# Kernel optimization log

Hardware: AMD Instinct MI355X
Metric: run time of the kernel (lower is better)

## Reference

```python
import jax, jax.numpy as jnp
import numpy as np

B, T, D_IN = 256, 2048, 64
H1, H2, D_OUT = 256, 256, 2


def setup_inputs() -> dict:
    key = jax.random.key(0)
    ks = jax.random.split(key, 12)
    s = lambda fan_in: 1.0 / np.sqrt(fan_in)
    u = lambda k, shape, b: jax.random.uniform(k, shape, jnp.float32, -b, b)
    return {
        "input_tensor": jax.random.normal(ks[0], (B, T, D_IN), jnp.float32),
        # layer 0 LSTMCell params (torch layout: [4H, in], gate order i,f,g,o)
        "W_ih0": u(ks[1], (4 * H1, D_IN), s(H1)),
        "W_hh0": u(ks[2], (4 * H1, H1), s(H1)),
        "b_ih0": u(ks[3], (4 * H1,), s(H1)),
        "b_hh0": u(ks[4], (4 * H1,), s(H1)),
        # layer 1 LSTMCell params
        "W_ih1": u(ks[5], (4 * H2, H1), s(H2)),
        "W_hh1": u(ks[6], (4 * H2, H2), s(H2)),
        "b_ih1": u(ks[7], (4 * H2,), s(H2)),
        "b_hh1": u(ks[8], (4 * H2,), s(H2)),
        # dense head
        "W_dense": u(ks[9], (D_OUT, H2), s(H2)),
        "b_dense": u(ks[10], (D_OUT,), s(H2)),
    }


def _lstm_cell(x, h, c, W_ih, W_hh, b_ih, b_hh):
    # gates: [B, 4H]; torch gate order i, f, g, o
    g = x @ W_ih.T + h @ W_hh.T + (b_ih + b_hh)
    i, f, gg, o = jnp.split(g, 4, axis=-1)
    c_new = jax.nn.sigmoid(f) * c + jax.nn.sigmoid(i) * jnp.tanh(gg)
    h_new = jax.nn.sigmoid(o) * jnp.tanh(c_new)
    return h_new, c_new


def reference(input_tensor, W_ih0, W_hh0, b_ih0, b_hh0,
              W_ih1, W_hh1, b_ih1, b_hh1, W_dense, b_dense):
    b = input_tensor.shape[0]
    h0 = jnp.zeros((b, H1), input_tensor.dtype)
    c0 = jnp.zeros((b, H1), input_tensor.dtype)
    h1 = jnp.zeros((b, H2), input_tensor.dtype)
    c1 = jnp.zeros((b, H2), input_tensor.dtype)

    def step(carry, x_t):
        h0, c0, h1, c1 = carry
        h0, c0 = _lstm_cell(x_t, h0, c0, W_ih0, W_hh0, b_ih0, b_hh0)
        h1, c1 = _lstm_cell(h0, h1, c1, W_ih1, W_hh1, b_ih1, b_hh1)
        return (h0, c0, h1, c1), None

    xs = jnp.swapaxes(input_tensor, 0, 1)  # [T, B, D_IN]
    (h0, c0, h1, c1), _ = jax.lax.scan(step, (h0, c0, h1, c1), xs)
    # dropout_rate=0.0 -> identity; final_act_type='none' -> identity
    out = h1 @ W_dense.T + b_dense  # [B, D_OUT]
    return out
```

## Files before the change

### kernel.cpp

```cpp
#include <hip/hip_runtime.h>
#include <math.h>

#define TT 2048
#define DIN 64
#define HH 256

typedef __attribute__((ext_vector_type(8))) short bf16x8;
typedef __attribute__((ext_vector_type(4))) float f32x4;
typedef __attribute__((ext_vector_type(4))) unsigned u32x4;
typedef unsigned short u16;
typedef unsigned u32t;

#define XS_STR 72
#define HS_STR 264
#define GB_STR 36

#define OFF_XS_HI  0
#define OFF_XS_LO  (OFF_XS_HI + 32*XS_STR)
#define OFF_HS0_HI (OFF_XS_LO + 32*XS_STR)
#define OFF_HS0_LO (OFF_HS0_HI + 32*HS_STR)
#define OFF_HS1_HI (OFF_HS0_LO + 32*HS_STR)
#define OFF_HS1_LO (OFF_HS1_HI + 32*HS_STR)
#define OFF_W0LO   (OFF_HS1_LO + 32*HS_STR)
#define OFF_W1LO   (OFF_W0LO + 1280*8)
#define SH_SHORTS  (OFF_W1LO + 2048*8)
#define SH_BYTES   (SH_SHORTS*2)
#define LDS_BYTES  (SH_BYTES + 2368*4)

__device__ __forceinline__ u16 f2bf(float f){
    u32t u = __builtin_bit_cast(u32t, f);
    u += 0x7fffu + ((u >> 16) & 1u);
    return (u16)(u >> 16);
}
__device__ __forceinline__ float bf2f(u16 h){
    u32t u = ((u32t)h) << 16;
    return __builtin_bit_cast(float, u);
}
__device__ __forceinline__ float sigf(float v){ return 1.0f/(1.0f+__expf(-v)); }
__device__ __forceinline__ float tanh_fast(float v){
    float x = fminf(fmaxf(v, -20.f), 20.f);
    float t = __expf(2.f*x);
    return (t - 1.f) / (t + 1.f);
}

__device__ __forceinline__ void split8(float4 a, float4 b, bf16x8& hi, bf16x8& lo){
    float v[8] = {a.x,a.y,a.z,a.w,b.x,b.y,b.z,b.w};
    #pragma unroll
    for (int j=0;j<8;++j){
        u16 h = f2bf(v[j]);
        hi[j] = (short)h;
        lo[j] = (short)f2bf(v[j] - bf2f(h));
    }
}

__device__ __forceinline__ void group_barrier(u32t* flg, int ug, unsigned epoch){
    __syncthreads();
    if (threadIdx.x == 0){
        asm volatile("s_waitcnt vmcnt(0)" ::: "memory");
        *(volatile u32t*)(flg + ug*16) = epoch;
    }
    if (threadIdx.x < 32){
        while (*(volatile u32t*)(flg + threadIdx.x*16) < epoch)
            __builtin_amdgcn_s_sleep(1);
    }
    __syncthreads();
}

#define MFMA16(a,b,c_) __builtin_amdgcn_mfma_f32_16x16x32_bf16(a,b,c_,0,0,0)

__global__ __launch_bounds__(256, 1)
void lstm_v8(const float* __restrict__ x,
             const float* __restrict__ Wih0, const float* __restrict__ Whh0,
             const float* __restrict__ bih0, const float* __restrict__ bhh0,
             const float* __restrict__ Wih1, const float* __restrict__ Whh1,
             const float* __restrict__ bih1, const float* __restrict__ bhh1,
             const float* __restrict__ Wd,   const float* __restrict__ bd,
             float* __restrict__ out, u16* __restrict__ hb,
             u32t* __restrict__ flags)
{
    extern __shared__ char smem[];
    short* sh  = (short*)smem;
    float* sf  = (float*)(smem + SH_BYTES);
    float* gb0 = sf;
    float* gb1 = sf + 1152;
    float* b0s = sf + 2304;
    float* b1s = sf + 2336;

    const int tid = threadIdx.x;
    const int w   = blockIdx.x;
    const int rb  = w & 7;
    const int ug  = w >> 3;
    const int rbase = rb * 32;
    const int u0  = ug * 8;

    u32t* flg = flags + rb * 512;


    const int l  = tid & 63;
    const int wv = tid >> 6;
    const int mt = wv >> 1, nt = wv & 1;
    const int c  = l & 15, ks = l >> 4;
    const int gbx = nt*2 + (c >> 3);
    const int g   = gbx*HH + u0 + (c & 7);

    bf16x8 w0h[10];
    #pragma unroll
    for (int kt = 0; kt < 10; ++kt) {
        int k = kt*32 + ks*8;
        const float* p = (k < 64) ? (Wih0 + (size_t)g*64 + k)
                                  : (Whh0 + (size_t)g*HH + (k - 64));
        bf16x8 hi_, lo_;
        split8(*(const float4*)p, *(const float4*)(p+4), hi_, lo_);
        w0h[kt] = hi_;
    }
    bf16x8 w1h[16];
    #pragma unroll
    for (int kt = 0; kt < 16; ++kt) {
        int k = kt*32 + ks*8;
        const float* p = (k < 256) ? (Wih1 + (size_t)g*HH + k)
                                   : (Whh1 + (size_t)g*HH + (k - 256));
        bf16x8 hi_, lo_;
        split8(*(const float4*)p, *(const float4*)(p+4), hi_, lo_);
        w1h[kt] = hi_;
    }
    for (int f = tid; f < 1280; f += 256) {
        int c_ = f & 15, ks_ = (f>>4)&3, nt_ = (f>>6)&1, kt_ = f>>7;
        int g_ = (nt_*2 + (c_>>3))*HH + u0 + (c_&7);
        int k_ = kt_*32 + ks_*8;
        const float* p = (k_ < 64) ? (Wih0 + (size_t)g_*64 + k_)
                                   : (Whh0 + (size_t)g_*HH + (k_ - 64));
        bf16x8 hi_, lo_;
        split8(*(const float4*)p, *(const float4*)(p+4), hi_, lo_);
        *(bf16x8*)(sh + OFF_W0LO + f*8) = lo_;
    }
    for (int f = tid; f < 2048; f += 256) {
        int c_ = f & 15, ks_ = (f>>4)&3, nt_ = (f>>6)&1, kt_ = f>>7;
        int g_ = (nt_*2 + (c_>>3))*HH + u0 + (c_&7);
        int k_ = kt_*32 + ks_*8;
        const float* p = (k_ < 256) ? (Wih1 + (size_t)g_*HH + k_)
                                    : (Whh1 + (size_t)g_*HH + (k_ - 256));
        bf16x8 hi_, lo_;
        split8(*(const float4*)p, *(const float4*)(p+4), hi_, lo_);
        *(bf16x8*)(sh + OFF_W1LO + f*8) = lo_;
    }

    if (tid < 32) {
        int gg_ = (tid >> 3)*HH + u0 + (tid & 7);
        b0s[tid] = bih0[gg_] + bhh0[gg_];
        b1s[tid] = bih1[gg_] + bhh1[gg_];
    }
    {
        int zr = tid >> 3, zu = tid & 7;
        size_t off = (size_t)(rbase + zr)*HH + u0 + zu;
        *(volatile u16*)(hb + off) = 0;          *(volatile u16*)(hb + 65536 + off) = 0;
        *(volatile u16*)(hb + 131072 + off) = 0; *(volatile u16*)(hb + 196608 + off) = 0;
        *(volatile u16*)(hb + 262144 + off) = 0; *(volatile u16*)(hb + 327680 + off) = 0;
        *(volatile u16*)(hb + 393216 + off) = 0; *(volatile u16*)(hb + 458752 + off) = 0;
    }
    {
        int xr = tid >> 3, xk = (tid & 7)*8;
        const float* xp = x + (size_t)(rbase + xr)*(TT*DIN) + xk;
        bf16x8 xh, xl;
        split8(*(const float4*)xp, *(const float4*)(xp+4), xh, xl);
        *(bf16x8*)(sh + OFF_XS_HI + xr*XS_STR + xk) = xh;
        *(bf16x8*)(sh + OFF_XS_LO + xr*XS_STR + xk) = xl;
    }
    group_barrier(flg, ug, 1u);

    const short* axh = sh + OFF_XS_HI  + (mt*16 + c)*XS_STR + ks*8;
    const short* axl = sh + OFF_XS_LO  + (mt*16 + c)*XS_STR + ks*8;
    const short* a0h = sh + OFF_HS0_HI + (mt*16 + c)*HS_STR + ks*8;
    const short* a0l = sh + OFF_HS0_LO + (mt*16 + c)*HS_STR + ks*8;
    const short* a1h = sh + OFF_HS1_HI + (mt*16 + c)*HS_STR + ks*8;
    const short* a1l = sh + OFF_HS1_LO + (mt*16 + c)*HS_STR + ks*8;
    const short* b0lo = sh + OFF_W0LO + (nt*64 + ks*16 + c)*8;
    const short* b1lo = sh + OFF_W1LO + (nt*64 + ks*16 + c)*8;
    float* gw0 = gb0 + (mt*16 + ks*4)*GB_STR + nt*16 + c;
    float* gw1 = gb1 + (mt*16 + ks*4)*GB_STR + nt*16 + c;
    const int ur = tid >> 3, uu = tid & 7;
    const size_t poff = (size_t)(rbase + ur)*HH + u0 + uu;

    float c0s = 0.f, c1s = 0.f;

    for (int k = 0; k <= TT; ++k) {
        {
            const unsigned rdo = ((k + 1) & 1) * 65536u;
            const u16* s0h = hb + rdo;
            const u16* s0l = hb + 131072 + rdo;
            const u16* s1h = hb + 262144 + rdo;
            const u16* s1l = hb + 393216 + rdo;
            #pragma unroll
            for (int j = 0; j < 4; ++j) {
                int cid = tid + j*256;
                int hr = cid >> 5, hk = (cid & 31)*8;
                size_t goff = (size_t)(rbase + hr)*HH + hk;
                int loff = hr*HS_STR + hk;
                *(u32x4*)(sh + OFF_HS0_HI + loff) = *(const volatile u32x4*)(s0h + goff);
                *(u32x4*)(sh + OFF_HS0_LO + loff) = *(const volatile u32x4*)(s0l + goff);
                *(u32x4*)(sh + OFF_HS1_HI + loff) = *(const volatile u32x4*)(s1h + goff);
                *(u32x4*)(sh + OFF_HS1_LO + loff) = *(const volatile u32x4*)(s1l + goff);
            }
        }
        __syncthreads();

        if (k < TT) {
            f32x4 ac[4] = {};
            #pragma unroll
            for (int kt = 0; kt < 10; ++kt) {
                const short* ph = (kt < 2) ? (axh + kt*32) : (a0h + (kt-2)*32);
                const short* pl = (kt < 2) ? (axl + kt*32) : (a0l + (kt-2)*32);
                bf16x8 ah = *(const bf16x8*)ph;
                bf16x8 al = *(const bf16x8*)pl;
                bf16x8 wl = *(const bf16x8*)(b0lo + kt*1024);
                const int q = kt & 3;
                ac[q] = MFMA16(ah, w0h[kt], ac[q]);
                ac[q] = MFMA16(al, w0h[kt], ac[q]);
                ac[q] = MFMA16(ah, wl,      ac[q]);
            }
            f32x4 aa = (ac[0] + ac[1]) + (ac[2] + ac[3]);
            gw0[0]        = aa[0];
            gw0[GB_STR]   = aa[1];
            gw0[2*GB_STR] = aa[2];
            gw0[3*GB_STR] = aa[3];
        }
        if (k >= 1) {
            f32x4 ac[4] = {};
            #pragma unroll
            for (int kt = 0; kt < 16; ++kt) {
                const short* ph = (kt < 8) ? (a0h + kt*32) : (a1h + (kt-8)*32);
                const short* pl = (kt < 8) ? (a0l + kt*32) : (a1l + (kt-8)*32);
                bf16x8 ah = *(const bf16x8*)ph;
                bf16x8 al = *(const bf16x8*)pl;
                bf16x8 wl = *(const bf16x8*)(b1lo + kt*1024);
                const int q = kt & 3;
                ac[q] = MFMA16(ah, w1h[kt], ac[q]);
                ac[q] = MFMA16(al, w1h[kt], ac[q]);
                ac[q] = MFMA16(ah, wl,      ac[q]);
            }
            f32x4 aa = (ac[0] + ac[1]) + (ac[2] + ac[3]);
            gw1[0]        = aa[0];
            gw1[GB_STR]   = aa[1];
            gw1[2*GB_STR] = aa[2];
            gw1[3*GB_STR] = aa[3];
        }
        __syncthreads();

        const unsigned wro = (k & 1) * 65536u;
        if (k < TT) {
            float gi = gb0[ur*GB_STR + uu]      + b0s[uu];
            float gf = gb0[ur*GB_STR + 8 + uu]  + b0s[8+uu];
            float gg = gb0[ur*GB_STR + 16 + uu] + b0s[16+uu];
            float go = gb0[ur*GB_STR + 24 + uu] + b0s[24+uu];
            c0s = sigf(gf)*c0s + sigf(gi)*tanh_fast(gg);
            float hn = sigf(go)*tanh_fast(c0s);
            u16 hh_ = f2bf(hn);
            u16 hl_ = f2bf(hn - bf2f(hh_));
            *(volatile u16*)(hb + wro + poff)          = hh_;
            *(volatile u16*)(hb + 131072 + wro + poff) = hl_;
        }
        if (k >= 1) {
            float gi = gb1[ur*GB_STR + uu]      + b1s[uu];
            float gf = gb1[ur*GB_STR + 8 + uu]  + b1s[8+uu];
            float gg = gb1[ur*GB_STR + 16 + uu] + b1s[16+uu];
            float go = gb1[ur*GB_STR + 24 + uu] + b1s[24+uu];
            c1s = sigf(gf)*c1s + sigf(gi)*tanh_fast(gg);
            float hn = sigf(go)*tanh_fast(c1s);
            u16 hh_ = f2bf(hn);
            u16 hl_ = f2bf(hn - bf2f(hh_));
            *(volatile u16*)(hb + 262144 + wro + poff) = hh_;
            *(volatile u16*)(hb + 393216 + wro + poff) = hl_;
        }
        if (k + 1 < TT) {
            int xr = tid >> 3, xk = (tid & 7)*8;
            const float* xp = x + (size_t)(rbase + xr)*(TT*DIN) + (size_t)(k+1)*DIN + xk;
            bf16x8 xh, xl;
            split8(*(const float4*)xp, *(const float4*)(xp+4), xh, xl);
            *(bf16x8*)(sh + OFF_XS_HI + xr*XS_STR + xk) = xh;
            *(bf16x8*)(sh + OFF_XS_LO + xr*XS_STR + xk) = xl;
        }
        group_barrier(flg, ug, (unsigned)(k+2));
    }

    if (ug == 0 && tid < 64) {
        int r = tid >> 1, j = tid & 1;
        const u16* hhp = hb + 262144 + (size_t)(rbase + r)*HH;
        const u16* hlp = hb + 393216 + (size_t)(rbase + r)*HH;
        const float* wdp = Wd + j*HH;
        float a = bd[j];
        #pragma unroll 4
        for (int q = 0; q < HH; ++q)
            a += (bf2f(*(const volatile u16*)(hhp + q)) +
                  bf2f(*(const volatile u16*)(hlp + q))) * wdp[q];
        out[(rbase + r)*2 + j] = a;
    }
}

extern "C" void kernel_launch(void* const* d_in, const int* in_sizes, int n_in,
                              void* d_out, int out_size, void* d_ws, size_t ws_size,
                              hipStream_t stream) {
    const float* x    = (const float*)d_in[0];
    const float* Wih0 = (const float*)d_in[1];
    const float* Whh0 = (const float*)d_in[2];
    const float* bih0 = (const float*)d_in[3];
    const float* bhh0 = (const float*)d_in[4];
    const float* Wih1 = (const float*)d_in[5];
    const float* Whh1 = (const float*)d_in[6];
    const float* bih1 = (const float*)d_in[7];
    const float* bhh1 = (const float*)d_in[8];
    const float* Wd   = (const float*)d_in[9];
    const float* bd   = (const float*)d_in[10];
    float* out = (float*)d_out;

    u32t* flags = (u32t*)d_ws;
    u16* hb = (u16*)((char*)d_ws + 32768);

    hipMemsetAsync(d_ws, 0, 32768, stream);

    hipFuncSetAttribute((const void*)lstm_v8,
                        hipFuncAttributeMaxDynamicSharedMemorySize, LDS_BYTES);

    lstm_v8<<<dim3(256), dim3(256), LDS_BYTES, stream>>>(
        x, Wih0, Whh0, bih0, bhh0, Wih1, Whh1, bih1, bhh1,
        Wd, bd, out, hb, flags);
}
```

Before: 17.00 ms.

## Use fragment-ordered hidden-state exchange layout, register-resident layer-1 weights, atomic barrier

```diff
diff --git a/kernel.cpp b/kernel.cpp
--- a/kernel.cpp
+++ b/kernel.cpp
@@ -11,21 +11,15 @@
 typedef unsigned short u16;
 typedef unsigned u32t;
 
-#define XS_STR 72
-#define HS_STR 264
-#define GB_STR 36
-
-#define OFF_XS_HI  0
-#define OFF_XS_LO  (OFF_XS_HI + 32*XS_STR)
-#define OFF_HS0_HI (OFF_XS_LO + 32*XS_STR)
-#define OFF_HS0_LO (OFF_HS0_HI + 32*HS_STR)
-#define OFF_HS1_HI (OFF_HS0_LO + 32*HS_STR)
-#define OFF_HS1_LO (OFF_HS1_HI + 32*HS_STR)
-#define OFF_W0LO   (OFF_HS1_LO + 32*HS_STR)
-#define OFF_W1LO   (OFF_W0LO + 1280*8)
-#define SH_SHORTS  (OFF_W1LO + 2048*8)
-#define SH_BYTES   (SH_SHORTS*2)
-#define LDS_BYTES  (SH_BYTES + 2368*4)
+#define LH0HI 0
+#define LH0LO 8192
+#define LH1HI 16384
+#define LH1LO 24576
+#define LX    32768
+#define LW0LO 40960
+#define SH_SHORTS 51200
+#define SH_BYTES (SH_SHORTS*2)
+#define LDS_BYTES (SH_BYTES + 2176*4)
 
 __device__ __forceinline__ u16 f2bf(float f){
     u32t u = __builtin_bit_cast(u32t, f);
@@ -42,7 +36,6 @@
     float t = __expf(2.f*x);
     return (t - 1.f) / (t + 1.f);
 }
-
 __device__ __forceinline__ void split8(float4 a, float4 b, bf16x8& hi, bf16x8& lo){
     float v[8] = {a.x,a.y,a.z,a.w,b.x,b.y,b.z,b.w};
     #pragma unroll
@@ -55,12 +48,10 @@
 
 __device__ __forceinline__ void group_barrier(u32t* flg, int ug, unsigned epoch){
     __syncthreads();
-    if (threadIdx.x == 0){
-        asm volatile("s_waitcnt vmcnt(0)" ::: "memory");
-        *(volatile u32t*)(flg + ug*16) = epoch;
-    }
+    if (threadIdx.x == 0)
+        __hip_atomic_store(flg + ug*16, epoch, __ATOMIC_RELEASE, __HIP_MEMORY_SCOPE_AGENT);
     if (threadIdx.x < 32){
-        while (*(volatile u32t*)(flg + threadIdx.x*16) < epoch)
+        while (__hip_atomic_load(flg + threadIdx.x*16, __ATOMIC_ACQUIRE, __HIP_MEMORY_SCOPE_AGENT) < epoch)
             __builtin_amdgcn_s_sleep(1);
     }
     __syncthreads();
@@ -69,22 +60,22 @@
 #define MFMA16(a,b,c_) __builtin_amdgcn_mfma_f32_16x16x32_bf16(a,b,c_,0,0,0)
 
 __global__ __launch_bounds__(256, 1)
-void lstm_v8(const float* __restrict__ x,
-             const float* __restrict__ Wih0, const float* __restrict__ Whh0,
-             const float* __restrict__ bih0, const float* __restrict__ bhh0,
-             const float* __restrict__ Wih1, const float* __restrict__ Whh1,
-             const float* __restrict__ bih1, const float* __restrict__ bhh1,
-             const float* __restrict__ Wd,   const float* __restrict__ bd,
-             float* __restrict__ out, u16* __restrict__ hb,
-             u32t* __restrict__ flags)
+void lstm_v11(const float* __restrict__ x,
+              const float* __restrict__ Wih0, const float* __restrict__ Whh0,
+              const float* __restrict__ bih0, const float* __restrict__ bhh0,
+              const float* __restrict__ Wih1, const float* __restrict__ Whh1,
+              const float* __restrict__ bih1, const float* __restrict__ bhh1,
+              const float* __restrict__ Wd,   const float* __restrict__ bd,
+              float* __restrict__ out, u16* __restrict__ hb,
+              u32t* __restrict__ flags)
 {
     extern __shared__ char smem[];
     short* sh  = (short*)smem;
     float* sf  = (float*)(smem + SH_BYTES);
-    float* gb0 = sf;
-    float* gb1 = sf + 1152;
-    float* b0s = sf + 2304;
-    float* b1s = sf + 2336;
+    float* gbT0 = sf;
+    float* gbT1 = sf + 1056;
+    float* b0s  = sf + 2112;
+    float* b1s  = sf + 2144;
 
     const int tid = threadIdx.x;
     const int w   = blockIdx.x;
@@ -95,6 +86,7 @@
 
     u32t* flg = flags + rb * 512;
 
+    u16* gbase = hb + (size_t)rb * 65536;
 
     const int l  = tid & 63;
     const int wv = tid >> 6;
@@ -105,112 +97,95 @@
 
     bf16x8 w0h[10];
     #pragma unroll
-    for (int kt = 0; kt < 10; ++kt) {
+    for (int kt = 0; kt < 10; ++kt){
         int k = kt*32 + ks*8;
-        const float* p = (k < 64) ? (Wih0 + (size_t)g*64 + k)
+        const float* p = (k < 64) ? (Wih0 + (size_t)g*DIN + k)
                                   : (Whh0 + (size_t)g*HH + (k - 64));
-        bf16x8 hi_, lo_;
-        split8(*(const float4*)p, *(const float4*)(p+4), hi_, lo_);
+        bf16x8 hi_, lo_; split8(*(const float4*)p, *(const float4*)(p+4), hi_, lo_);
         w0h[kt] = hi_;
     }
-    bf16x8 w1h[16];
+    bf16x8 w1h[16], w1l[16];
     #pragma unroll
-    for (int kt = 0; kt < 16; ++kt) {
+    for (int kt = 0; kt < 16; ++kt){
         int k = kt*32 + ks*8;
         const float* p = (k < 256) ? (Wih1 + (size_t)g*HH + k)
                                    : (Whh1 + (size_t)g*HH + (k - 256));
-        bf16x8 hi_, lo_;
-        split8(*(const float4*)p, *(const float4*)(p+4), hi_, lo_);
-        w1h[kt] = hi_;
-    }
-    for (int f = tid; f < 1280; f += 256) {
+        bf16x8 hi_, lo_; split8(*(const float4*)p, *(const float4*)(p+4), hi_, lo_);
+        w1h[kt] = hi_; w1l[kt] = lo_;
+    }
+    for (int f = tid; f < 1280; f += 256){
         int c_ = f & 15, ks_ = (f>>4)&3, nt_ = (f>>6)&1, kt_ = f>>7;
         int g_ = (nt_*2 + (c_>>3))*HH + u0 + (c_&7);
         int k_ = kt_*32 + ks_*8;
-        const float* p = (k_ < 64) ? (Wih0 + (size_t)g_*64 + k_)
+        const float* p = (k_ < 64) ? (Wih0 + (size_t)g_*DIN + k_)
                                    : (Whh0 + (size_t)g_*HH + (k_ - 64));
-        bf16x8 hi_, lo_;
-        split8(*(const float4*)p, *(const float4*)(p+4), hi_, lo_);
-        *(bf16x8*)(sh + OFF_W0LO + f*8) = lo_;
-    }
-    for (int f = tid; f < 2048; f += 256) {
-        int c_ = f & 15, ks_ = (f>>4)&3, nt_ = (f>>6)&1, kt_ = f>>7;
-        int g_ = (nt_*2 + (c_>>3))*HH + u0 + (c_&7);
-        int k_ = kt_*32 + ks_*8;
-        const float* p = (k_ < 256) ? (Wih1 + (size_t)g_*HH + k_)
-                                    : (Whh1 + (size_t)g_*HH + (k_ - 256));
-        bf16x8 hi_, lo_;
-        split8(*(const float4*)p, *(const float4*)(p+4), hi_, lo_);
-        *(bf16x8*)(sh + OFF_W1LO + f*8) = lo_;
-    }
-
-    if (tid < 32) {
-        int gg_ = (tid >> 3)*HH + u0 + (tid & 7);
+        bf16x8 hi_, lo_; split8(*(const float4*)p, *(const float4*)(p+4), hi_, lo_);
+        *(bf16x8*)(sh + LW0LO + f*8) = lo_;
+    }
+
+    if (tid < 32){
+        int gg_ = ((tid>>4)*2 + ((tid>>3)&1))*HH + u0 + (tid & 7);
         b0s[tid] = bih0[gg_] + bhh0[gg_];
         b1s[tid] = bih1[gg_] + bhh1[gg_];
     }
     {
-        int zr = tid >> 3, zu = tid & 7;
-        size_t off = (size_t)(rbase + zr)*HH + u0 + zu;
-        *(volatile u16*)(hb + off) = 0;          *(volatile u16*)(hb + 65536 + off) = 0;
-        *(volatile u16*)(hb + 131072 + off) = 0; *(volatile u16*)(hb + 196608 + off) = 0;
-        *(volatile u16*)(hb + 262144 + off) = 0; *(volatile u16*)(hb + 327680 + off) = 0;
-        *(volatile u16*)(hb + 393216 + off) = 0; *(volatile u16*)(hb + 458752 + off) = 0;
+        int idx = ug*256 + tid;
+        u32x4 z = {0u,0u,0u,0u};
+        *(u32x4*)(gbase + (size_t)idx*8) = z;
     }
     {
-        int xr = tid >> 3, xk = (tid & 7)*8;
-        const float* xp = x + (size_t)(rbase + xr)*(TT*DIN) + xk;
-        bf16x8 xh, xl;
-        split8(*(const float4*)xp, *(const float4*)(xp+4), xh, xl);
-        *(bf16x8*)(sh + OFF_XS_HI + xr*XS_STR + xk) = xh;
-        *(bf16x8*)(sh + OFF_XS_LO + xr*XS_STR + xk) = xl;
+        int xr = tid >> 3, k8 = tid & 7;
+        const float* xp = x + (size_t)(rbase + xr)*(TT*DIN) + k8*8;
+        bf16x8 xh, xl; split8(*(const float4*)xp, *(const float4*)(xp+4), xh, xl);
+        short* d = sh + LX + (k8>>2)*1024 + (xr>>4)*512
+                 + (((k8&3) ^ (xr&3))<<7) + (xr&15)*8;
+        *(bf16x8*)d = xh;
+        *(bf16x8*)(d + 2048) = xl;
     }
     group_barrier(flg, ug, 1u);
 
-    const short* axh = sh + OFF_XS_HI  + (mt*16 + c)*XS_STR + ks*8;
-    const short* axl = sh + OFF_XS_LO  + (mt*16 + c)*XS_STR + ks*8;
-    const short* a0h = sh + OFF_HS0_HI + (mt*16 + c)*HS_STR + ks*8;
-    const short* a0l = sh + OFF_HS0_LO + (mt*16 + c)*HS_STR + ks*8;
-    const short* a1h = sh + OFF_HS1_HI + (mt*16 + c)*HS_STR + ks*8;
-    const short* a1l = sh + OFF_HS1_LO + (mt*16 + c)*HS_STR + ks*8;
-    const short* b0lo = sh + OFF_W0LO + (nt*64 + ks*16 + c)*8;
-    const short* b1lo = sh + OFF_W1LO + (nt*64 + ks*16 + c)*8;
-    float* gw0 = gb0 + (mt*16 + ks*4)*GB_STR + nt*16 + c;
-    float* gw1 = gb1 + (mt*16 + ks*4)*GB_STR + nt*16 + c;
+    const int hoff = mt*512 + l*8;
+    const int xoff = mt*512 + ((ks ^ (c&3))<<7) + c*8;
+    const short* b0lo = sh + LW0LO + (nt*64 + ks*16 + c)*8;
+    float* gw0 = gbT0 + (nt*16 + c)*33 + mt*16 + ks*4;
+    float* gw1 = gbT1 + (nt*16 + c)*33 + mt*16 + ks*4;
+
     const int ur = tid >> 3, uu = tid & 7;
-    const size_t poff = (size_t)(rbase + ur)*HH + u0 + uu;
+    const int fpub = (ug>>2)*1024 + (ur>>4)*512 + ((ug&3)<<7) + (ur&15)*8 + uu;
 
     float c0s = 0.f, c1s = 0.f;
 
-    for (int k = 0; k <= TT; ++k) {
+    for (int k = 0; k <= TT; ++k){
         {
-            const unsigned rdo = ((k + 1) & 1) * 65536u;
-            const u16* s0h = hb + rdo;
-            const u16* s0l = hb + 131072 + rdo;
-            const u16* s1h = hb + 262144 + rdo;
-            const u16* s1l = hb + 393216 + rdo;
+            const int p = (k + 1) & 1;
+            const u16* s0h = gbase + (0 + p)*8192;
+            const u16* s0l = gbase + (2 + p)*8192;
+            const u16* s1h = gbase + (4 + p)*8192;
+            const u16* s1l = gbase + (6 + p)*8192;
             #pragma unroll
-            for (int j = 0; j < 4; ++j) {
-                int cid = tid + j*256;
-                int hr = cid >> 5, hk = (cid & 31)*8;
-                size_t goff = (size_t)(rbase + hr)*HH + hk;
-                int loff = hr*HS_STR + hk;
-                *(u32x4*)(sh + OFF_HS0_HI + loff) = *(const volatile u32x4*)(s0h + goff);
-                *(u32x4*)(sh + OFF_HS0_LO + loff) = *(const volatile u32x4*)(s0l + goff);
-                *(u32x4*)(sh + OFF_HS1_HI + loff) = *(const volatile u32x4*)(s1h + goff);
-                *(u32x4*)(sh + OFF_HS1_LO + loff) = *(const volatile u32x4*)(s1l + goff);
+            for (int j = 0; j < 4; ++j){
+                int idx = (tid + j*256) * 8;
+                *(u32x4*)(sh + LH0HI + idx) = *(const u32x4*)(s0h + idx);
+                *(u32x4*)(sh + LH0LO + idx) = *(const u32x4*)(s0l + idx);
+                *(u32x4*)(sh + LH1HI + idx) = *(const u32x4*)(s1h + idx);
+                *(u32x4*)(sh + LH1LO + idx) = *(const u32x4*)(s1l + idx);
             }
         }
         __syncthreads();
 
-        if (k < TT) {
+        if (k < TT){
             f32x4 ac[4] = {};
+            const short* xb = sh + LX + (k&1)*4096 + xoff;
             #pragma unroll
-            for (int kt = 0; kt < 10; ++kt) {
-                const short* ph = (kt < 2) ? (axh + kt*32) : (a0h + (kt-2)*32);
-                const short* pl = (kt < 2) ? (axl + kt*32) : (a0l + (kt-2)*32);
-                bf16x8 ah = *(const bf16x8*)ph;
-                bf16x8 al = *(const bf16x8*)pl;
+            for (int kt = 0; kt < 10; ++kt){
+                bf16x8 ah, al;
+                if (kt < 2){
+                    ah = *(const bf16x8*)(xb + kt*1024);
+                    al = *(const bf16x8*)(xb + kt*1024 + 2048);
+                } else {
+                    ah = *(const bf16x8*)(sh + LH0HI + (kt-2)*1024 + hoff);
+                    al = *(const bf16x8*)(sh + LH0LO + (kt-2)*1024 + hoff);
+                }
                 bf16x8 wl = *(const bf16x8*)(b0lo + kt*1024);
                 const int q = kt & 3;
                 ac[q] = MFMA16(ah, w0h[kt], ac[q]);
@@ -218,79 +193,76 @@
                 ac[q] = MFMA16(ah, wl,      ac[q]);
             }
             f32x4 aa = (ac[0] + ac[1]) + (ac[2] + ac[3]);
-            gw0[0]        = aa[0];
-            gw0[GB_STR]   = aa[1];
-            gw0[2*GB_STR] = aa[2];
-            gw0[3*GB_STR] = aa[3];
-        }
-        if (k >= 1) {
+            *(float4*)gw0 = (float4){aa[0], aa[1], aa[2], aa[3]};
+        }
+        if (k >= 1){
             f32x4 ac[4] = {};
             #pragma unroll
-            for (int kt = 0; kt < 16; ++kt) {
-                const short* ph = (kt < 8) ? (a0h + kt*32) : (a1h + (kt-8)*32);
-                const short* pl = (kt < 8) ? (a0l + kt*32) : (a1l + (kt-8)*32);
-                bf16x8 ah = *(const bf16x8*)ph;
-                bf16x8 al = *(const bf16x8*)pl;
-                bf16x8 wl = *(const bf16x8*)(b1lo + kt*1024);
+            for (int kt = 0; kt < 16; ++kt){
+                bf16x8 ah, al;
+                if (kt < 8){
+                    ah = *(const bf16x8*)(sh + LH0HI + kt*1024 + hoff);
+                    al = *(const bf16x8*)(sh + LH0LO + kt*1024 + hoff);
+                } else {
+                    ah = *(const bf16x8*)(sh + LH1HI + (kt-8)*1024 + hoff);
+                    al = *(const bf16x8*)(sh + LH1LO + (kt-8)*1024 + hoff);
+                }
                 const int q = kt & 3;
                 ac[q] = MFMA16(ah, w1h[kt], ac[q]);
                 ac[q] = MFMA16(al, w1h[kt], ac[q]);
-                ac[q] = MFMA16(ah, wl,      ac[q]);
+                ac[q] = MFMA16(ah, w1l[kt], ac[q]);
             }
             f32x4 aa = (ac[0] + ac[1]) + (ac[2] + ac[3]);
-            gw1[0]        = aa[0];
-            gw1[GB_STR]   = aa[1];
-            gw1[2*GB_STR] = aa[2];
-            gw1[3*GB_STR] = aa[3];
+            *(float4*)gw1 = (float4){aa[0], aa[1], aa[2], aa[3]};
         }
         __syncthreads();
 
-        const unsigned wro = (k & 1) * 65536u;
-        if (k < TT) {
-            float gi = gb0[ur*GB_STR + uu]      + b0s[uu];
-            float gf = gb0[ur*GB_STR + 8 + uu]  + b0s[8+uu];
-            float gg = gb0[ur*GB_STR + 16 + uu] + b0s[16+uu];
-            float go = gb0[ur*GB_STR + 24 + uu] + b0s[24+uu];
+        const int pw = (k & 1);
+        if (k < TT){
+            float gi = gbT0[(uu   )*33 + ur] + b0s[uu];
+            float gf = gbT0[(8+uu )*33 + ur] + b0s[8+uu];
+            float gg = gbT0[(16+uu)*33 + ur] + b0s[16+uu];
+            float go = gbT0[(24+uu)*33 + ur] + b0s[24+uu];
             c0s = sigf(gf)*c0s + sigf(gi)*tanh_fast(gg);
             float hn = sigf(go)*tanh_fast(c0s);
-            u16 hh_ = f2bf(hn);
-            u16 hl_ = f2bf(hn - bf2f(hh_));
-            *(volatile u16*)(hb + wro + poff)          = hh_;
-            *(volatile u16*)(hb + 131072 + wro + poff) = hl_;
-        }
-        if (k >= 1) {
-            float gi = gb1[ur*GB_STR + uu]      + b1s[uu];
-            float gf = gb1[ur*GB_STR + 8 + uu]  + b1s[8+uu];
-            float gg = gb1[ur*GB_STR + 16 + uu] + b1s[16+uu];
-            float go = gb1[ur*GB_STR + 24 + uu] + b1s[24+uu];
+            u16 hh_ = f2bf(hn), hl_ = f2bf(hn - bf2f(hh_));
+            gbase[(0 + pw)*8192 + fpub] = hh_;
+            gbase[(2 + pw)*8192 + fpub] = hl_;
+        }
+        if (k >= 1){
+            float gi = gbT1[(uu   )*33 + ur] + b1s[uu];
+            float gf = gbT1[(8+uu )*33 + ur] + b1s[8+uu];
+            float gg = gbT1[(16+uu)*33 + ur] + b1s[16+uu];
+            float go = gbT1[(24+uu)*33 + ur] + b1s[24+uu];
             c1s = sigf(gf)*c1s + sigf(gi)*tanh_fast(gg);
             float hn = sigf(go)*tanh_fast(c1s);
-            u16 hh_ = f2bf(hn);
-            u16 hl_ = f2bf(hn - bf2f(hh_));
-            *(volatile u16*)(hb + 262144 + wro + poff) = hh_;
-            *(volatile u16*)(hb + 393216 + wro + poff) = hl_;
-        }
-        if (k + 1 < TT) {
-            int xr = tid >> 3, xk = (tid & 7)*8;
-            const float* xp = x + (size_t)(rbase + xr)*(TT*DIN) + (size_t)(k+1)*DIN + xk;
-            bf16x8 xh, xl;
-            split8(*(const float4*)xp, *(const float4*)(xp+4), xh, xl);
-            *(bf16x8*)(sh + OFF_XS_HI + xr*XS_STR + xk) = xh;
-            *(bf16x8*)(sh + OFF_XS_LO + xr*XS_STR + xk) = xl;
-        }
-        group_barrier(flg, ug, (unsigned)(k+2));
-    }
-
-    if (ug == 0 && tid < 64) {
+            u16 hh_ = f2bf(hn), hl_ = f2bf(hn - bf2f(hh_));
+            gbase[(4 + pw)*8192 + fpub] = hh_;
+            gbase[(6 + pw)*8192 + fpub] = hl_;
+        }
+        if (k + 1 < TT){
+            int xr = tid >> 3, k8 = tid & 7;
+            const float* xp = x + (size_t)(rbase + xr)*(TT*DIN) + (size_t)(k+1)*DIN + k8*8;
+            bf16x8 xh, xl; split8(*(const float4*)xp, *(const float4*)(xp+4), xh, xl);
+            short* d = sh + LX + ((k+1)&1)*4096 + (k8>>2)*1024 + (xr>>4)*512
+                     + (((k8&3) ^ (xr&3))<<7) + (xr&15)*8;
+            *(bf16x8*)d = xh;
+            *(bf16x8*)(d + 2048) = xl;
+        }
+        group_barrier(flg, ug, (unsigned)(k + 2));
+    }
+
+    if (ug == 0 && tid < 64){
         int r = tid >> 1, j = tid & 1;
-        const u16* hhp = hb + 262144 + (size_t)(rbase + r)*HH;
-        const u16* hlp = hb + 393216 + (size_t)(rbase + r)*HH;
+        const u16* hh = gbase + 4*8192;
+        const u16* hl = gbase + 6*8192;
         const float* wdp = Wd + j*HH;
         float a = bd[j];
         #pragma unroll 4
-        for (int q = 0; q < HH; ++q)
-            a += (bf2f(*(const volatile u16*)(hhp + q)) +
-                  bf2f(*(const volatile u16*)(hlp + q))) * wdp[q];
+        for (int q = 0; q < HH; ++q){
+            int f = (q>>5)*1024 + (r>>4)*512 + (((q>>3)&3)<<7) + (r&15)*8 + (q&7);
+            a += (bf2f(hh[f]) + bf2f(hl[f])) * wdp[q];
+        }
         out[(rbase + r)*2 + j] = a;
     }
 }
@@ -316,10 +288,10 @@
 
     hipMemsetAsync(d_ws, 0, 32768, stream);
 
-    hipFuncSetAttribute((const void*)lstm_v8,
+    hipFuncSetAttribute((const void*)lstm_v11,
                         hipFuncAttributeMaxDynamicSharedMemorySize, LDS_BYTES);
 
-    lstm_v8<<<dim3(256), dim3(256), LDS_BYTES, stream>>>(
+    lstm_v11<<<dim3(256), dim3(256), LDS_BYTES, stream>>>(
         x, Wih0, Whh0, bih0, bhh0, Wih1, Whh1, bih1, bhh1,
         Wd, bd, out, hb, flags);
 }
```

New measurement: 21.37 ms. +25.7%, slower.
